# Kernel tuning notes

Measured on AMD Instinct MI355X. Metric: run time of the kernel, lower is better.

Reference implementation:

```python
import jax, jax.numpy as jnp
import numpy as np

N_NODES = 50000
N_EDGES = 400000
D = 64          # in/out channels (residual forces equality)
H = 8           # attention heads
L = 3           # number of GATv2 layers
NEG_SLOPE = 0.2
LN_EPS = 1e-5


def setup_inputs() -> dict:
    key = jax.random.key(0)
    ks = jax.random.split(key, 6)
    x = jax.random.normal(ks[0], (N_NODES, D), dtype=jnp.float32)
    edge_index = jax.random.randint(ks[1], (2, N_EDGES), 0, N_NODES, dtype=jnp.int64)
    scale = 1.0 / np.sqrt(D)
    Wl = jax.random.normal(ks[2], (L, D, H * D), dtype=jnp.float32) * scale
    Wr = jax.random.normal(ks[3], (L, D, H * D), dtype=jnp.float32) * scale
    att = jax.random.normal(ks[4], (L, H, D), dtype=jnp.float32) * 0.1
    b = jnp.zeros((L, D), dtype=jnp.float32)
    gamma = jnp.ones((L, D), dtype=jnp.float32)
    beta = jnp.zeros((L, D), dtype=jnp.float32)
    return {"x": x, "Wl": Wl, "Wr": Wr, "att": att, "b": b,
            "gamma": gamma, "beta": beta, "edge_index": edge_index}


def _gatv2_stack(x, Wl, Wr, att, b, gamma, beta, src, dst, num_nodes):
    # src/dst already include self-loops (PyG add_self_loops=True)
    for l in range(Wl.shape[0]):
        xl = (x @ Wl[l]).reshape(num_nodes, H, -1)   # [N,H,C] messages (source transform)
        xr = (x @ Wr[l]).reshape(num_nodes, H, -1)   # [N,H,C] target transform
        m = jax.nn.leaky_relu(xl[src] + xr[dst], NEG_SLOPE)       # [E,H,C]
        e = jnp.einsum('ehc,hc->eh', m, att[l])                    # [E,H]
        # segment softmax over incoming edges of each target node
        emax = jax.ops.segment_max(e, dst, num_segments=num_nodes)
        ex = jnp.exp(e - emax[dst])
        denom = jax.ops.segment_sum(ex, dst, num_segments=num_nodes)
        alpha = ex / denom[dst]                                    # [E,H]
        agg = jax.ops.segment_sum(alpha[:, :, None] * xl[src], dst,
                                  num_segments=num_nodes)          # [N,H,C]
        h = agg.mean(axis=1) + b[l]                                # concat=False -> head mean, + bias
        x = h + x                                                  # residual
        mu = x.mean(-1, keepdims=True)
        var = x.var(-1, keepdims=True)
        x = (x - mu) / jnp.sqrt(var + LN_EPS) * gamma[l] + beta[l] # LayerNorm
        x = jax.nn.relu(x)
    return x


def reference(x, Wl, Wr, att, b, gamma, beta, edge_index):
    num_nodes = x.shape[0]
    loops = jnp.arange(num_nodes, dtype=edge_index.dtype)
    src = jnp.concatenate([edge_index[0], loops])
    dst = jnp.concatenate([edge_index[1], loops])
    return _gatv2_stack(x, Wl, Wr, att, b, gamma, beta, src, dst, num_nodes)
```

## Files before the change

kernel.cpp:

```cpp
#include <hip/hip_runtime.h>

#define N_NODES 50000
#define N_EDGES 400000
#define EP (N_EDGES + N_NODES)
#define D 64
#define H 8
#define NEG_SLOPE 0.2f
#define LN_EPS 1e-5f
#define CHUNK 196
#define SCAN_BLOCKS 256
#define PAD_N 50048

typedef unsigned short ushort_t;
typedef unsigned int uint_t;
typedef __attribute__((ext_vector_type(8))) short short8;
typedef __attribute__((ext_vector_type(4))) float f32x4;
typedef __attribute__((ext_vector_type(2))) float f32x2;

#if defined(__has_builtin)
#if __has_builtin(__builtin_amdgcn_cvt_pk_bf16_f32)
#define HAVE_CVT_PK_BF16 1
#endif
#endif

__device__ __forceinline__ ushort_t f2bf(float f) {
    uint_t u = __float_as_uint(f);
    u += 0x7fffu + ((u >> 16) & 1u);
    return (ushort_t)(u >> 16);
}
__device__ __forceinline__ uint_t pack_bf2(float a, float b) {
#ifdef HAVE_CVT_PK_BF16
    typedef __attribute__((ext_vector_type(2))) __bf16 bf16x2_t;
    bf16x2_t v = __builtin_amdgcn_cvt_pk_bf16_f32(a, b);
    uint_t r;
    __builtin_memcpy(&r, &v, 4);
    return r;
#else
    return (uint_t)f2bf(a) | ((uint_t)f2bf(b) << 16);
#endif
}
__device__ __forceinline__ f32x2 mkf2(uint_t u) {
    f32x2 r;
    r.x = __uint_as_float(u << 16);
    r.y = __uint_as_float(u & 0xffff0000u);
    return r;
}
__device__ __forceinline__ f32x2 absf2(f32x2 a) {
    f32x2 r;
    r.x = __uint_as_float(__float_as_uint(a.x) & 0x7fffffffu);
    r.y = __uint_as_float(__float_as_uint(a.y) & 0x7fffffffu);
    return r;
}

__device__ __forceinline__ void edge_sd(const int* __restrict__ ei, int eid, int& s, int& d) {
    if (eid < N_EDGES) { s = ei[eid]; d = ei[N_EDGES + eid]; }
    else               { s = d = eid - N_EDGES; }
}


__global__ __launch_bounds__(256) void setup_all(const int* __restrict__ ei, int* __restrict__ counts,
                                                 const float* __restrict__ x,
                                                 const float* __restrict__ Wl, const float* __restrict__ Wr,
                                                 ushort_t* __restrict__ xb, ushort_t* __restrict__ Wt) {
    int t = blockIdx.x * 256 + threadIdx.x;
    if (t < EP) {
        int s, d; edge_sd(ei, t, s, d);
        atomicAdd(&counts[d], 1);
        return;
    }
    t -= EP;
    if (t < N_NODES * 64) { xb[t] = f2bf(x[t]); return; }
    t -= N_NODES * 64;
    if (t >= 3 * 1024 * 64) return;
    int l = t >> 16, rem = t & 65535, col = rem >> 6, k = rem & 63;
    float v = (col < 512) ? Wl[((size_t)l * 64 + k) * 512 + col]
                          : Wr[((size_t)l * 64 + k) * 512 + (col - 512)];
    Wt[t] = f2bf(v);
}


__global__ __launch_bounds__(256) void csr_scan1(const int* __restrict__ counts, int* __restrict__ bsum) {
    __shared__ int sd[256];
    int t = threadIdx.x, b = blockIdx.x;
    int idx = b * CHUNK + t;
    sd[t] = (t < CHUNK && idx < N_NODES) ? counts[idx] : 0;
    __syncthreads();
    for (int d = 128; d > 0; d >>= 1) {
        if (t < d) sd[t] += sd[t + d];
        __syncthreads();
    }
    if (t == 0) bsum[b] = sd[0];
}

__global__ __launch_bounds__(256) void csr_scan2(int* __restrict__ bsum) {
    __shared__ int sd[256];
    int t = threadIdx.x;
    sd[t] = bsum[t];
    __syncthreads();
    for (int d = 1; d < 256; d <<= 1) {
        int v = (t >= d) ? sd[t - d] : 0;
        __syncthreads();
        if (t >= d) sd[t] += v;
        __syncthreads();
    }
    bsum[t] = (t > 0) ? sd[t - 1] : 0;
}

__global__ __launch_bounds__(256) void csr_scan3(const int* __restrict__ counts, const int* __restrict__ bsum,
                                                 int* __restrict__ offsets, int* __restrict__ cursor,
                                                 int* __restrict__ bhist) {
    __shared__ int sd[256];
    __shared__ int hist[64];
    int t = threadIdx.x, b = blockIdx.x;
    if (t < 64) hist[t] = 0;
    int idx = b * CHUNK + t;
    int v = (t < CHUNK && idx < N_NODES) ? counts[idx] : 0;
    sd[t] = v;
    __syncthreads();
    for (int d = 1; d < 256; d <<= 1) {
        int u = (t >= d) ? sd[t - d] : 0;
        __syncthreads();
        if (t >= d) sd[t] += u;
        __syncthreads();
    }
    if (t < CHUNK && idx < N_NODES) {
        int ex = bsum[b] + sd[t] - v;
        offsets[idx] = ex;
        cursor[idx]  = ex;
        atomicAdd(&hist[63 - min(v, 63)], 1);
    }
    __syncthreads();
    if (t < 64) bhist[b * 64 + t] = hist[t];
    if (b == 0 && t == 0) offsets[N_NODES] = EP;
}

__global__ void deg_scan(const int* __restrict__ bhist, int* __restrict__ pbase) {
    __shared__ int tot[64], base[64];
    int t = threadIdx.x;
    if (t < 64) {
        int s = 0;
        for (int b = 0; b < SCAN_BLOCKS; ++b) s += bhist[b * 64 + t];
        tot[t] = s;
    }
    __syncthreads();
    if (t == 0) {
        int run = 0;
        for (int k = 0; k < 64; ++k) { base[k] = run; run += tot[k]; }
    }
    __syncthreads();
    if (t < 64) {
        int run = base[t];
        for (int b = 0; b < SCAN_BLOCKS; ++b) { pbase[b * 64 + t] = run; run += bhist[b * 64 + t]; }
    }
}

__global__ __launch_bounds__(256) void place_scatter(const int* __restrict__ counts, const int* __restrict__ pbase,
                                                     int* __restrict__ node_order,
                                                     const int* __restrict__ ei, int* __restrict__ cursor,
                                                     int* __restrict__ csr_src) {
    int b = blockIdx.x;
    if (b < SCAN_BLOCKS) {
        __shared__ int cur[64];
        int t = threadIdx.x;
        if (t < 64) cur[t] = pbase[b * 64 + t];
        __syncthreads();
        int idx = b * CHUNK + t;
        if (t < CHUNK && idx < N_NODES) {
            int bin = 63 - min(counts[idx], 63);
            int p = atomicAdd(&cur[bin], 1);
            node_order[p] = idx;
        }
    } else {
        int t = (b - SCAN_BLOCKS) * 256 + threadIdx.x;
        if (t >= EP) return;
        int s, d; edge_sd(ei, t, s, d);
        int pos = atomicAdd(&cursor[d], 1);
        csr_src[pos] = s;
    }
}

__global__ __launch_bounds__(256) void gemm_mfma(const ushort_t* __restrict__ xb,
                                                 const ushort_t* __restrict__ Wt,
                                                 ushort_t* __restrict__ xlr) {
    __shared__ ushort_t sW[128 * 72];
    int t = threadIdx.x;
    int colq = blockIdx.y;
    const ushort_t* Wg = Wt + (size_t)colq * 128 * 64;
    {
        int col = t >> 1, half = t & 1;
        const uint4* g = (const uint4*)(Wg + col * 64 + half * 32);
        uint4* l = (uint4*)(sW + col * 72 + half * 32);
        l[0] = g[0]; l[1] = g[1]; l[2] = g[2]; l[3] = g[3];
    }
    __syncthreads();
    int lane = t & 63, w = t >> 6;
    int ln = lane & 15, q = lane >> 4;
    int node = blockIdx.x * 64 + w * 16 + ln;
    int nclamp = node < N_NODES ? node : N_NODES - 1;
    const short8 b0 = *(const short8*)(xb + (size_t)nclamp * 64 + q * 8);
    const short8 b1 = *(const short8*)(xb + (size_t)nclamp * 64 + 32 + q * 8);
#pragma unroll
    for (int ct = 0; ct < 8; ++ct) {
        const short8 a0 = *(const short8*)(sW + (ct * 16 + ln) * 72 + q * 8);
        const short8 a1 = *(const short8*)(sW + (ct * 16 + ln) * 72 + 32 + q * 8);
        f32x4 acc = {0.f, 0.f, 0.f, 0.f};
        acc = __builtin_amdgcn_mfma_f32_16x16x32_bf16(a0, b0, acc, 0, 0, 0);
        acc = __builtin_amdgcn_mfma_f32_16x16x32_bf16(a1, b1, acc, 0, 0, 0);
        if (node < N_NODES) {
            uint_t lo = pack_bf2(acc[0], acc[1]);
            uint_t hi = pack_bf2(acc[2], acc[3]);
            *(uint2*)(xlr + (size_t)node * 1024 + colq * 128 + ct * 16 + q * 4) = make_uint2(lo, hi);
        }
    }
}

__global__ __launch_bounds__(256) void node_fused(const float* __restrict__ x_in,
                                                  const ushort_t* __restrict__ xlr,
                                                  const float* __restrict__ att,
                                                  const int* __restrict__ offsets, const int* __restrict__ csr_src,
                                                  const int* __restrict__ node_order,
                                                  const float* __restrict__ bias, const float* __restrict__ gamma,
                                                  const float* __restrict__ beta, float* __restrict__ x_out,
                                                  ushort_t* __restrict__ xb_out) {
    int n = node_order[blockIdx.x * 4 + (threadIdx.x >> 6)];
    n = __builtin_amdgcn_readfirstlane(n);
    int lane = threadIdx.x & 63;
    int h = lane >> 3, i = lane & 7;
    int beg = __builtin_amdgcn_readfirstlane(offsets[n]);
    int end = __builtin_amdgcn_readfirstlane(offsets[n + 1]);
    int off = h * 64 + i * 8;

    uint4 ru = *(const uint4*)(xlr + (size_t)n * 1024 + 512 + off);
    f32x2 rv0 = mkf2(ru.x), rv1 = mkf2(ru.y), rv2 = mkf2(ru.z), rv3 = mkf2(ru.w);
    const float4* pa = (const float4*)(att + h * 64 + i * 8);
    float4 aa = pa[0], ab = pa[1];
    f32x2 a0 = {aa.x, aa.y}, a1 = {aa.z, aa.w}, a2 = {ab.x, ab.y}, a3 = {ab.z, ab.w};
    f32x2 a60 = 0.6f * a0, a61 = 0.6f * a1, a62 = 0.6f * a2, a63 = 0.6f * a3;
    f32x2 a40 = 0.4f * a0, a41 = 0.4f * a1, a42 = 0.4f * a2, a43 = 0.4f * a3;

    float den = 0.f;
    f32x2 acc0 = {0.f, 0.f}, acc1 = {0.f, 0.f}, acc2 = {0.f, 0.f}, acc3 = {0.f, 0.f};

#define PROCESS(cur)                                                     \
    {                                                                    \
        f32x2 v0 = mkf2(cur.x), v1 = mkf2(cur.y),                        \
              v2 = mkf2(cur.z), v3 = mkf2(cur.w);                        \
        f32x2 p = a60 * v0;                                              \
        p = a61 * v1 + p;                                                \
        p = a62 * v2 + p;                                                \
        p = a63 * v3 + p;                                                \
        p = a40 * absf2(v0 + rv0) + p;                                   \
        p = a41 * absf2(v1 + rv1) + p;                                   \
        p = a42 * absf2(v2 + rv2) + p;                                   \
        p = a43 * absf2(v3 + rv3) + p;                                   \
        float pdot = p.x + p.y;                                          \
        pdot += __shfl_xor(pdot, 1);                                     \
        pdot += __shfl_xor(pdot, 2);                                     \
        pdot += __shfl_xor(pdot, 4);                                     \
        float wgt = __expf(pdot);                                        \
        den += wgt;                                                      \
        f32x2 wv = {wgt, wgt};                                           \
        acc0 = wv * v0 + acc0;                                           \
        acc1 = wv * v1 + acc1;                                           \
        acc2 = wv * v2 + acc2;                                           \
        acc3 = wv * v3 + acc3;                                           \
    }

    for (int base = beg; base < end; base += 64) {
        int idx = base + lane;
        int srcs = csr_src[idx < end ? idx : end - 1];
        int cnt = min(64, end - base);
        int j = 0;
        for (; j + 8 <= cnt; j += 8) {
            uint4 q[8];
#pragma unroll
            for (int u = 0; u < 8; ++u) {
                int ss = __shfl(srcs, j + u);
                q[u] = *(const uint4*)(xlr + (size_t)ss * 1024 + off);
            }
#pragma unroll
            for (int u = 0; u < 8; ++u) PROCESS(q[u]);
        }
        for (; j < cnt; ++j) {
            int ss = __shfl(srcs, j);
            uint4 qq = *(const uint4*)(xlr + (size_t)ss * 1024 + off);
            PROCESS(qq);
        }
    }
#undef PROCESS

    float invden = 0.125f / den;
    f32x2 iv = {invden, invden};
    acc0 *= iv; acc1 *= iv; acc2 *= iv; acc3 *= iv;
    float acc[8] = {acc0.x, acc0.y, acc1.x, acc1.y, acc2.x, acc2.y, acc3.x, acc3.y};
#pragma unroll
    for (int dm = 8; dm < 64; dm <<= 1) {
#pragma unroll
        for (int k2 = 0; k2 < 8; ++k2) acc[k2] += __shfl_xor(acc[k2], dm);
    }

    int cbase = i * 8;
    const float4* px = (const float4*)(x_in + n * 64 + cbase);
    float4 x0 = px[0], x1 = px[1];
    float xi[8] = {x0.x, x0.y, x0.z, x0.w, x1.x, x1.y, x1.z, x1.w};
    float v[8];
    float sum = 0.f, sq = 0.f;
#pragma unroll
    for (int k2 = 0; k2 < 8; ++k2) {
        float val = acc[k2] + bias[cbase + k2] + xi[k2];
        v[k2] = val; sum += val; sq += val * val;
    }
#pragma unroll
    for (int dm = 1; dm < 8; dm <<= 1) { sum += __shfl_xor(sum, dm); sq += __shfl_xor(sq, dm); }
    float mu   = sum * (1.0f / 64.0f);
    float var  = sq * (1.0f / 64.0f) - mu * mu;
    float rstd = rsqrtf(var + LN_EPS);

    if (h == 0) {
        float o[8];
#pragma unroll
        for (int k2 = 0; k2 < 8; ++k2) {
            float y = (v[k2] - mu) * rstd * gamma[cbase + k2] + beta[cbase + k2];
            o[k2] = fmaxf(y, 0.f);
        }
        float4* po = (float4*)(x_out + n * 64 + cbase);
        po[0] = make_float4(o[0], o[1], o[2], o[3]);
        po[1] = make_float4(o[4], o[5], o[6], o[7]);
        *(uint4*)(xb_out + (size_t)n * 64 + cbase) =
            make_uint4(pack_bf2(o[0], o[1]), pack_bf2(o[2], o[3]),
                       pack_bf2(o[4], o[5]), pack_bf2(o[6], o[7]));
    }
}


extern "C" void kernel_launch(void* const* d_in, const int* in_sizes, int n_in,
                              void* d_out, int out_size, void* d_ws, size_t ws_size,
                              hipStream_t stream) {
    const float* x     = (const float*)d_in[0];
    const float* Wl    = (const float*)d_in[1];
    const float* Wr    = (const float*)d_in[2];
    const float* att   = (const float*)d_in[3];
    const float* b     = (const float*)d_in[4];
    const float* gamma = (const float*)d_in[5];
    const float* beta  = (const float*)d_in[6];
    const int*   ei    = (const int*)d_in[7];
    float* out = (float*)d_out;

    ushort_t* xlr = (ushort_t*)d_ws;
    ushort_t* xb  = xlr + (size_t)N_NODES * 1024;
    ushort_t* Wt  = xb + (size_t)PAD_N * 64;
    int* counts     = (int*)(Wt + 3 * 1024 * 64);
    int* offsets    = counts + PAD_N;
    int* cursor     = offsets + PAD_N;
    int* bsum       = cursor + PAD_N;
    int* node_order = bsum + 256;
    int* bhist      = node_order + PAD_N;
    int* pbase      = bhist + SCAN_BLOCKS * 64;
    int* csr_src    = pbase + SCAN_BLOCKS * 64;

    hipMemsetAsync(counts, 0, N_NODES * sizeof(int), stream);

    int setup_threads = EP + N_NODES * 64 + 3 * 1024 * 64;
    setup_all<<<(setup_threads + 255) / 256, 256, 0, stream>>>(ei, counts, x, Wl, Wr, xb, Wt);

    csr_scan1<<<SCAN_BLOCKS, 256, 0, stream>>>(counts, bsum);
    csr_scan2<<<1, 256, 0, stream>>>(bsum);
    csr_scan3<<<SCAN_BLOCKS, 256, 0, stream>>>(counts, bsum, offsets, cursor, bhist);
    deg_scan <<<1, 256, 0, stream>>>(bhist, pbase);
    int eb = (EP + 255) / 256;
    place_scatter<<<SCAN_BLOCKS + eb, 256, 0, stream>>>(counts, pbase, node_order, ei, cursor, csr_src);

    const float* xin = x;
    dim3 ggrid(PAD_N / 64, 8);
    for (int l = 0; l < 3; ++l) {
        gemm_mfma <<<ggrid, 256, 0, stream>>>(xb, Wt + (size_t)l * 1024 * 64, xlr);
        node_fused<<<N_NODES / 4, 256, 0, stream>>>(xin, xlr, att + l * (H * D), offsets, csr_src,
                                                    node_order, b + l * D, gamma + l * D, beta + l * D,
                                                    out, xb);
        xin = out;
    }
}
```

Before: 476.0 us.

## Merge CSR build kernels, fuse edge scatter into first GEMM, use DPP reductions

Moves the degree histogram into the first scan kernel and folds the degree-bin prefix into the single-block scan. Node ordering now happens in the third scan, which removes two kernel launches. The CSR edge scatter runs as extra blocks of the layer-0 GEMM launch, so it can overlap with the matrix multiply. Cross-lane shuffles in the attention and LayerNorm reductions are replaced with DPP and ds_swizzle intrinsics, which adds some risk of wrong lane patterns.

```diff
diff --git a/kernel.cpp b/kernel.cpp
--- a/kernel.cpp
+++ b/kernel.cpp
@@ -10,6 +10,7 @@
 #define CHUNK 196
 #define SCAN_BLOCKS 256
 #define PAD_N 50048
+#define GEMM_BLOCKS (782 * 8)
 
 typedef unsigned short ushort_t;
 typedef unsigned int uint_t;
@@ -52,6 +53,25 @@
     return r;
 }
 
+__device__ __forceinline__ float xor1_dpp(float x) {
+    int i = __float_as_int(x);
+    return __int_as_float(__builtin_amdgcn_update_dpp(i, i, 0xB1, 0xF, 0xF, 1));
+}
+__device__ __forceinline__ float xor2_dpp(float x) {
+    int i = __float_as_int(x);
+    return __int_as_float(__builtin_amdgcn_update_dpp(i, i, 0x4E, 0xF, 0xF, 1));
+}
+__device__ __forceinline__ float xor8_dpp(float x) {
+    int i = __float_as_int(x);
+    return __int_as_float(__builtin_amdgcn_update_dpp(i, i, 0x128, 0xF, 0xF, 1));
+}
+__device__ __forceinline__ float xor4_swz(float x) {
+    return __int_as_float(__builtin_amdgcn_ds_swizzle(__float_as_int(x), 0x101F));
+}
+__device__ __forceinline__ float xor16_swz(float x) {
+    return __int_as_float(__builtin_amdgcn_ds_swizzle(__float_as_int(x), 0x401F));
+}
+
 __device__ __forceinline__ void edge_sd(const int* __restrict__ ei, int eid, int& s, int& d) {
     if (eid < N_EDGES) { s = ei[eid]; d = ei[N_EDGES + eid]; }
     else               { s = d = eid - N_EDGES; }
@@ -79,35 +99,7 @@
 }
 
 
-__global__ __launch_bounds__(256) void csr_scan1(const int* __restrict__ counts, int* __restrict__ bsum) {
-    __shared__ int sd[256];
-    int t = threadIdx.x, b = blockIdx.x;
-    int idx = b * CHUNK + t;
-    sd[t] = (t < CHUNK && idx < N_NODES) ? counts[idx] : 0;
-    __syncthreads();
-    for (int d = 128; d > 0; d >>= 1) {
-        if (t < d) sd[t] += sd[t + d];
-        __syncthreads();
-    }
-    if (t == 0) bsum[b] = sd[0];
-}
-
-__global__ __launch_bounds__(256) void csr_scan2(int* __restrict__ bsum) {
-    __shared__ int sd[256];
-    int t = threadIdx.x;
-    sd[t] = bsum[t];
-    __syncthreads();
-    for (int d = 1; d < 256; d <<= 1) {
-        int v = (t >= d) ? sd[t - d] : 0;
-        __syncthreads();
-        if (t >= d) sd[t] += v;
-        __syncthreads();
-    }
-    bsum[t] = (t > 0) ? sd[t - 1] : 0;
-}
-
-__global__ __launch_bounds__(256) void csr_scan3(const int* __restrict__ counts, const int* __restrict__ bsum,
-                                                 int* __restrict__ offsets, int* __restrict__ cursor,
+__global__ __launch_bounds__(256) void csr_scan1(const int* __restrict__ counts, int* __restrict__ bsum,
                                                  int* __restrict__ bhist) {
     __shared__ int sd[256];
     __shared__ int hist[64];
@@ -117,6 +109,65 @@
     int v = (t < CHUNK && idx < N_NODES) ? counts[idx] : 0;
     sd[t] = v;
     __syncthreads();
+    if (t < CHUNK && idx < N_NODES) atomicAdd(&hist[63 - min(v, 63)], 1);
+    for (int d = 128; d > 0; d >>= 1) {
+        __syncthreads();
+        if (t < d) sd[t] += sd[t + d];
+    }
+    __syncthreads();
+    if (t == 0) bsum[b] = sd[0];
+    if (t < 64) bhist[b * 64 + t] = hist[t];
+}
+
+__global__ __launch_bounds__(256) void csr_scan2(int* __restrict__ bsum,
+                                                 const int* __restrict__ bhist, int* __restrict__ pbase) {
+    __shared__ int sd[256];
+    __shared__ int sg[64 * 4];
+    __shared__ int base[64];
+    int t = threadIdx.x;
+    sd[t] = bsum[t];
+    __syncthreads();
+    for (int d = 1; d < 256; d <<= 1) {
+        int v = (t >= d) ? sd[t - d] : 0;
+        __syncthreads();
+        if (t >= d) sd[t] += v;
+        __syncthreads();
+    }
+    bsum[t] = (t > 0) ? sd[t - 1] : 0;
+
+    int k = t & 63, g = t >> 6;
+    int s = 0;
+    for (int j = 0; j < 64; ++j) s += bhist[(g * 64 + j) * 64 + k];
+    sg[k * 4 + g] = s;
+    __syncthreads();
+    if (t == 0) {
+        int run = 0;
+        for (int kk = 0; kk < 64; ++kk) {
+            base[kk] = run;
+            run += sg[kk * 4 + 0] + sg[kk * 4 + 1] + sg[kk * 4 + 2] + sg[kk * 4 + 3];
+        }
+    }
+    __syncthreads();
+    int run = base[k];
+    for (int gg = 0; gg < g; ++gg) run += sg[k * 4 + gg];
+    for (int j = 0; j < 64; ++j) {
+        int b = g * 64 + j;
+        pbase[b * 64 + k] = run;
+        run += bhist[b * 64 + k];
+    }
+}
+
+__global__ __launch_bounds__(256) void csr_scan3(const int* __restrict__ counts, const int* __restrict__ bsum,
+                                                 int* __restrict__ offsets, int* __restrict__ cursor,
+                                                 const int* __restrict__ pbase, int* __restrict__ node_order) {
+    __shared__ int sd[256];
+    __shared__ int cur[64];
+    int t = threadIdx.x, b = blockIdx.x;
+    if (t < 64) cur[t] = pbase[b * 64 + t];
+    int idx = b * CHUNK + t;
+    int v = (t < CHUNK && idx < N_NODES) ? counts[idx] : 0;
+    sd[t] = v;
+    __syncthreads();
     for (int d = 1; d < 256; d <<= 1) {
         int u = (t >= d) ? sd[t - d] : 0;
         __syncthreads();
@@ -127,64 +178,31 @@
         int ex = bsum[b] + sd[t] - v;
         offsets[idx] = ex;
         cursor[idx]  = ex;
-        atomicAdd(&hist[63 - min(v, 63)], 1);
-    }
-    __syncthreads();
-    if (t < 64) bhist[b * 64 + t] = hist[t];
+        int bin = 63 - min(v, 63);
+        int p = atomicAdd(&cur[bin], 1);
+        node_order[p] = idx;
+    }
     if (b == 0 && t == 0) offsets[N_NODES] = EP;
 }
 
-__global__ void deg_scan(const int* __restrict__ bhist, int* __restrict__ pbase) {
-    __shared__ int tot[64], base[64];
-    int t = threadIdx.x;
-    if (t < 64) {
-        int s = 0;
-        for (int b = 0; b < SCAN_BLOCKS; ++b) s += bhist[b * 64 + t];
-        tot[t] = s;
-    }
-    __syncthreads();
-    if (t == 0) {
-        int run = 0;
-        for (int k = 0; k < 64; ++k) { base[k] = run; run += tot[k]; }
-    }
-    __syncthreads();
-    if (t < 64) {
-        int run = base[t];
-        for (int b = 0; b < SCAN_BLOCKS; ++b) { pbase[b * 64 + t] = run; run += bhist[b * 64 + t]; }
-    }
-}
-
-__global__ __launch_bounds__(256) void place_scatter(const int* __restrict__ counts, const int* __restrict__ pbase,
-                                                     int* __restrict__ node_order,
-                                                     const int* __restrict__ ei, int* __restrict__ cursor,
-                                                     int* __restrict__ csr_src) {
+__global__ __launch_bounds__(256) void gemm_mfma(const ushort_t* __restrict__ xb,
+                                                 const ushort_t* __restrict__ Wt,
+                                                 ushort_t* __restrict__ xlr,
+                                                 const int* __restrict__ ei, int* __restrict__ cursor,
+                                                 int* __restrict__ csr_src) {
+    __shared__ ushort_t sW[128 * 72];
     int b = blockIdx.x;
-    if (b < SCAN_BLOCKS) {
-        __shared__ int cur[64];
-        int t = threadIdx.x;
-        if (t < 64) cur[t] = pbase[b * 64 + t];
-        __syncthreads();
-        int idx = b * CHUNK + t;
-        if (t < CHUNK && idx < N_NODES) {
-            int bin = 63 - min(counts[idx], 63);
-            int p = atomicAdd(&cur[bin], 1);
-            node_order[p] = idx;
-        }
-    } else {
-        int t = (b - SCAN_BLOCKS) * 256 + threadIdx.x;
+    if (b >= GEMM_BLOCKS) {
+        int t = (b - GEMM_BLOCKS) * 256 + threadIdx.x;
         if (t >= EP) return;
         int s, d; edge_sd(ei, t, s, d);
         int pos = atomicAdd(&cursor[d], 1);
         csr_src[pos] = s;
-    }
-}
-
-__global__ __launch_bounds__(256) void gemm_mfma(const ushort_t* __restrict__ xb,
-                                                 const ushort_t* __restrict__ Wt,
-                                                 ushort_t* __restrict__ xlr) {
-    __shared__ ushort_t sW[128 * 72];
+        return;
+    }
+    int colq = b / 782;
+    int bx = b - colq * 782;
     int t = threadIdx.x;
-    int colq = blockIdx.y;
     const ushort_t* Wg = Wt + (size_t)colq * 128 * 64;
     {
         int col = t >> 1, half = t & 1;
@@ -195,7 +213,7 @@
     __syncthreads();
     int lane = t & 63, w = t >> 6;
     int ln = lane & 15, q = lane >> 4;
-    int node = blockIdx.x * 64 + w * 16 + ln;
+    int node = bx * 64 + w * 16 + ln;
     int nclamp = node < N_NODES ? node : N_NODES - 1;
     const short8 b0 = *(const short8*)(xb + (size_t)nclamp * 64 + q * 8);
     const short8 b1 = *(const short8*)(xb + (size_t)nclamp * 64 + 32 + q * 8);
@@ -254,9 +272,9 @@
         p = a42 * absf2(v2 + rv2) + p;                                   \
         p = a43 * absf2(v3 + rv3) + p;                                   \
         float pdot = p.x + p.y;                                          \
-        pdot += __shfl_xor(pdot, 1);                                     \
-        pdot += __shfl_xor(pdot, 2);                                     \
-        pdot += __shfl_xor(pdot, 4);                                     \
+        pdot += xor1_dpp(pdot);                                          \
+        pdot += xor2_dpp(pdot);                                          \
+        pdot += xor4_swz(pdot);                                          \
         float wgt = __expf(pdot);                                        \
         den += wgt;                                                      \
         f32x2 wv = {wgt, wgt};                                           \
@@ -294,9 +312,10 @@
     acc0 *= iv; acc1 *= iv; acc2 *= iv; acc3 *= iv;
     float acc[8] = {acc0.x, acc0.y, acc1.x, acc1.y, acc2.x, acc2.y, acc3.x, acc3.y};
 #pragma unroll
-    for (int dm = 8; dm < 64; dm <<= 1) {
-#pragma unroll
-        for (int k2 = 0; k2 < 8; ++k2) acc[k2] += __shfl_xor(acc[k2], dm);
+    for (int k2 = 0; k2 < 8; ++k2) {
+        acc[k2] += xor8_dpp(acc[k2]);
+        acc[k2] += xor16_swz(acc[k2]);
+        acc[k2] += __shfl_xor(acc[k2], 32);
     }
 
     int cbase = i * 8;
@@ -310,8 +329,9 @@
         float val = acc[k2] + bias[cbase + k2] + xi[k2];
         v[k2] = val; sum += val; sq += val * val;
     }
-#pragma unroll
-    for (int dm = 1; dm < 8; dm <<= 1) { sum += __shfl_xor(sum, dm); sq += __shfl_xor(sq, dm); }
+    sum += xor1_dpp(sum); sq += xor1_dpp(sq);
+    sum += xor2_dpp(sum); sq += xor2_dpp(sq);
+    sum += xor4_swz(sum); sq += xor4_swz(sq);
     float mu   = sum * (1.0f / 64.0f);
     float var  = sq * (1.0f / 64.0f) - mu * mu;
     float rstd = rsqrtf(var + LN_EPS);
@@ -363,17 +383,15 @@
     int setup_threads = EP + N_NODES * 64 + 3 * 1024 * 64;
     setup_all<<<(setup_threads + 255) / 256, 256, 0, stream>>>(ei, counts, x, Wl, Wr, xb, Wt);
 
-    csr_scan1<<<SCAN_BLOCKS, 256, 0, stream>>>(counts, bsum);
-    csr_scan2<<<1, 256, 0, stream>>>(bsum);
-    csr_scan3<<<SCAN_BLOCKS, 256, 0, stream>>>(counts, bsum, offsets, cursor, bhist);
-    deg_scan <<<1, 256, 0, stream>>>(bhist, pbase);
+    csr_scan1<<<SCAN_BLOCKS, 256, 0, stream>>>(counts, bsum, bhist);
+    csr_scan2<<<1, 256, 0, stream>>>(bsum, bhist, pbase);
+    csr_scan3<<<SCAN_BLOCKS, 256, 0, stream>>>(counts, bsum, offsets, cursor, pbase, node_order);
+
     int eb = (EP + 255) / 256;
-    place_scatter<<<SCAN_BLOCKS + eb, 256, 0, stream>>>(counts, pbase, node_order, ei, cursor, csr_src);
-
     const float* xin = x;
-    dim3 ggrid(PAD_N / 64, 8);
     for (int l = 0; l < 3; ++l) {
-        gemm_mfma <<<ggrid, 256, 0, stream>>>(xb, Wt + (size_t)l * 1024 * 64, xlr);
+        int grid = (l == 0) ? GEMM_BLOCKS + eb : GEMM_BLOCKS;
+        gemm_mfma <<<grid, 256, 0, stream>>>(xb, Wt + (size_t)l * 1024 * 64, xlr, ei, cursor, csr_src);
         node_fused<<<N_NODES / 4, 256, 0, stream>>>(xin, xlr, att + l * (H * D), offsets, csr_src,
                                                     node_order, b + l * D, gamma + l * D, beta + l * D,
                                                     out, xb);
```

Result: faster. 466.4 us (-2.0%).
